# Optimization experiments

Hardware: AMD Instinct MI355X
Metric: run time of the kernel (lower is better)

The kernel has to match this reference:

```python
import jax, jax.numpy as jnp
import numpy as np

E = 1024
H = 16
D = E // H  # head_dim = 64
FF = 4 * E
EPS = 1e-5


def layernorm(x, g, b):
    mu = jnp.mean(x, axis=-1, keepdims=True)
    var = jnp.var(x, axis=-1, keepdims=True)
    return (x - mu) * jax.lax.rsqrt(var + EPS) * g + b


def setup_inputs() -> dict:
    key = jax.random.key(0)
    ks = jax.random.split(key, 12)
    s = 1.0 / np.sqrt(E)
    sf = 1.0 / np.sqrt(FF)
    return {
        "x": jax.random.normal(ks[0], (2, 2048, E), dtype=jnp.float32),
        "wq": jax.random.uniform(ks[1], (E, E), jnp.float32, -s, s),
        "wk": jax.random.uniform(ks[2], (E, E), jnp.float32, -s, s),
        "wv": jax.random.uniform(ks[3], (E, E), jnp.float32, -s, s),
        "wo": jax.random.uniform(ks[4], (E, E), jnp.float32, -s, s),
        "bo": jax.random.uniform(ks[5], (E,), jnp.float32, -s, s),
        "g1": jnp.ones((E,), jnp.float32),
        "b1": jnp.zeros((E,), jnp.float32),
        "w1": jax.random.uniform(ks[6], (FF, E), jnp.float32, -s, s),
        "bf1": jax.random.uniform(ks[7], (FF,), jnp.float32, -s, s),
        "w2": jax.random.uniform(ks[8], (E, FF), jnp.float32, -sf, sf),
        "bf2": jax.random.uniform(ks[9], (E,), jnp.float32, -sf, sf),
        "g2": jnp.ones((E,), jnp.float32),
        "b2": jnp.zeros((E,), jnp.float32),
    }


def reference(x, wq, wk, wv, wo, bo, g1, b1, w1, bf1, w2, bf2, g2, b2):
    B, L, _ = x.shape
    # projections (torch Linear: x @ W.T)
    q = (x @ wq.T).reshape(B, L, H, D).transpose(0, 2, 1, 3)  # (B,H,L,D)
    k = (x @ wk.T).reshape(B, L, H, D).transpose(0, 2, 1, 3)
    v = (x @ wv.T).reshape(B, L, H, D).transpose(0, 2, 1, 3)
    scores = jnp.einsum('bhqd,bhkd->bhqk', q, k) / np.sqrt(D)
    attn = jax.nn.softmax(scores, axis=-1)
    ctx = jnp.einsum('bhqk,bhkd->bhqd', attn, v)
    ctx = ctx.transpose(0, 2, 1, 3).reshape(B, L, E)
    attn_out = ctx @ wo.T + bo
    h = layernorm(x + attn_out, g1, b1)
    ff = jax.nn.gelu(h @ w1.T + bf1, approximate=False) @ w2.T + bf2
    return layernorm(h + ff, g2, b2)
```

## Files before the change

### kernel.cpp

```cpp
#include <hip/hip_runtime.h>
#include <hip/hip_bf16.h>
#include <stdint.h>

typedef __bf16 bf16x8 __attribute__((ext_vector_type(8)));
typedef float  f32x4  __attribute__((ext_vector_type(4)));
typedef unsigned short u16;
typedef u16 u16x8 __attribute__((ext_vector_type(8)));

__device__ __forceinline__ u16 f2b(float f) {
  uint32_t u = __builtin_bit_cast(uint32_t, f);
  u += 0x7fffu + ((u >> 16) & 1u);
  return (u16)(u >> 16);
}

__device__ __forceinline__ float b2f(u16 b) {
  uint32_t u = (uint32_t)b << 16;
  return __builtin_bit_cast(float, u);
}

__device__ __forceinline__ f32x4 mfma16(bf16x8 a, bf16x8 b, f32x4 c) {
  return __builtin_amdgcn_mfma_f32_16x16x32_bf16(a, b, c, 0, 0, 0);
}

__device__ __forceinline__ void gload_lds16(const void* g, void* l) {
  __builtin_amdgcn_global_load_lds(
      (const __attribute__((address_space(1))) void*)g,
      (__attribute__((address_space(3))) void*)l, 16, 0, 0);
}

__global__ void f2b_all(const float* __restrict__ x,  const float* __restrict__ wq,
                        const float* __restrict__ wk, const float* __restrict__ wv,
                        const float* __restrict__ wo, const float* __restrict__ w1,
                        const float* __restrict__ w2,
                        u16* __restrict__ xb, u16* __restrict__ wqkvb,
                        u16* __restrict__ wob, u16* __restrict__ w1b,
                        u16* __restrict__ w2b) {
  const int i = blockIdx.x * blockDim.x + threadIdx.x;
  const float* src; u16* dst; int off;
  if (i < 524288)        { src = x;  dst = xb;              off = i; }
  else if (i < 655360)   { src = wq; dst = wqkvb;           off = i - 524288; }
  else if (i < 786432)   { src = wk; dst = wqkvb + 1048576; off = i - 655360; }
  else if (i < 917504)   { src = wv; dst = wqkvb + 2097152; off = i - 786432; }
  else if (i < 1048576)  { src = wo; dst = wob;             off = i - 917504; }
  else if (i < 1572864)  { src = w1; dst = w1b;             off = i - 1048576; }
  else                   { src = w2; dst = w2b;             off = i - 1572864; }
  const float4* p = (const float4*)src + (size_t)off * 2;
  float4 a = p[0], b = p[1];
  u16x8 r;
  r[0] = f2b(a.x); r[1] = f2b(a.y); r[2] = f2b(a.z); r[3] = f2b(a.w);
  r[4] = f2b(b.x); r[5] = f2b(b.y); r[6] = f2b(b.z); r[7] = f2b(b.w);
  *((u16x8*)dst + off) = r;
}

template<int MODE>
__global__ __launch_bounds__(256, 4) void gemm_bt(
    const u16* __restrict__ A, const u16* __restrict__ W,
    const float* __restrict__ bias,
    void* __restrict__ o0, void* __restrict__ o1,
    void* __restrict__ o2, void* __restrict__ o3,
    int Nsz, int Kstride, int Klen, int ntiles)
{
  __shared__ u16 As[2][128 * 32];
  __shared__ u16 Bs[2][128 * 32];
  const int nbn = Nsz >> 7;
  int bid = blockIdx.x;
  bid = (bid & 7) * ((int)gridDim.x >> 3) + (bid >> 3);
  const int tile = (MODE == 1) ? (bid % ntiles) : bid;
  const int sid  = (MODE == 1) ? (bid / ntiles) : 0;
  const int koff = sid * Klen;
  const int bm = tile / nbn;
  const int bn = tile % nbn;
  const int tid = threadIdx.x;
  const int w = tid >> 6, l = tid & 63;
  const int lh = l >> 4, ll = l & 15;
  const int wr = w >> 1, wc = w & 1;

  f32x4 acc[4][4] = {};

  const u16* Ag = A + (size_t)(bm * 128) * Kstride + koff;
  const u16* Wg = W + (size_t)(bn * 128) * Kstride + koff;

  const int flat0 = (w * 2) * 64 + l;
  const int flat1 = (w * 2 + 1) * 64 + l;

  {
    gload_lds16(Ag + (size_t)(flat0 >> 2) * Kstride + (flat0 & 3) * 8, As[0] + flat0 * 8);
    gload_lds16(Wg + (size_t)(flat0 >> 2) * Kstride + (flat0 & 3) * 8, Bs[0] + flat0 * 8);
    gload_lds16(Ag + (size_t)(flat1 >> 2) * Kstride + (flat1 & 3) * 8, As[0] + flat1 * 8);
    gload_lds16(Wg + (size_t)(flat1 >> 2) * Kstride + (flat1 & 3) * 8, Bs[0] + flat1 * 8);
  }
  __syncthreads();

  const int NS = Klen >> 5;
  int buf = 0;
  for (int s = 0; s < NS; ++s) {
    if (s + 1 < NS) {
      const int k0 = (s + 1) * 32;
      gload_lds16(Ag + (size_t)(flat0 >> 2) * Kstride + k0 + (flat0 & 3) * 8, As[buf ^ 1] + flat0 * 8);
      gload_lds16(Wg + (size_t)(flat0 >> 2) * Kstride + k0 + (flat0 & 3) * 8, Bs[buf ^ 1] + flat0 * 8);
      gload_lds16(Ag + (size_t)(flat1 >> 2) * Kstride + k0 + (flat1 & 3) * 8, As[buf ^ 1] + flat1 * 8);
      gload_lds16(Wg + (size_t)(flat1 >> 2) * Kstride + k0 + (flat1 & 3) * 8, Bs[buf ^ 1] + flat1 * 8);
    }
    bf16x8 af[4], bfr[4];
#pragma unroll
    for (int mi = 0; mi < 4; ++mi)
      af[mi] = *(const bf16x8*)(As[buf] + (wr * 64 + mi * 16 + ll) * 32 + lh * 8);
#pragma unroll
    for (int ni = 0; ni < 4; ++ni)
      bfr[ni] = *(const bf16x8*)(Bs[buf] + (wc * 64 + ni * 16 + ll) * 32 + lh * 8);
    __builtin_amdgcn_s_setprio(1);
#pragma unroll
    for (int mi = 0; mi < 4; ++mi)
#pragma unroll
      for (int ni = 0; ni < 4; ++ni)
        acc[mi][ni] = mfma16(af[mi], bfr[ni], acc[mi][ni]);
    __builtin_amdgcn_s_setprio(0);
    __syncthreads();
    buf ^= 1;
  }

#pragma unroll
  for (int mi = 0; mi < 4; ++mi) {
#pragma unroll
    for (int ni = 0; ni < 4; ++ni) {
      const int col = bn * 128 + wc * 64 + ni * 16 + ll;
#pragma unroll
      for (int i = 0; i < 4; ++i) {
        const int row = bm * 128 + wr * 64 + mi * 16 + lh * 4 + i;
        float v = acc[mi][ni][i];
        if (MODE == 1) {
          u16* dst = (sid == 0) ? (u16*)o0 : (sid == 1) ? (u16*)o1
                   : (sid == 2) ? (u16*)o2 : (u16*)o3;
          dst[(size_t)row * Nsz + col] = f2b(v);
        } else if (MODE == 2) {
          float xx = v + bias[col];
          float u = xx * (0.7978845608f + 0.0356774081f * xx * xx);
          float t = __builtin_amdgcn_exp2f(u * 2.8853900818f);
          float r = __builtin_amdgcn_rcpf(1.0f + t);
          ((u16*)o0)[(size_t)row * Nsz + col] = f2b(xx * t * r);
        } else {
          const int which = col >> 10;
          const int e = col & 1023;
          const int hh = e >> 6, dd = e & 63;
          const int bb = row >> 11, nl = row & 2047;
          if (which == 0) {
            ((u16*)o0)[((size_t)(bb * 16 + hh) * 2048 + nl) * 64 + dd] = f2b(v * 0.18033688f);
          } else if (which == 1) {
            ((u16*)o1)[((size_t)(bb * 16 + hh) * 2048 + nl) * 64 + dd] = f2b(v);
          } else {
            ((u16*)o2)[((size_t)(bb * 16 + hh) * 64 + dd) * 2048 + nl] = f2b(v);
          }
        }
      }
    }
  }
}

__global__ __launch_bounds__(256, 2) void attn_fwd(
    const u16* __restrict__ Q, const u16* __restrict__ K,
    const u16* __restrict__ Vt, u16* __restrict__ ctx)
{
  __shared__ u16 Ks[3][64 * 64];
  __shared__ u16 Vs[3][64 * 64];
  __shared__ u16 Ps[4][32 * 64];

  const int bh = blockIdx.x & 31;
  const int qt = blockIdx.x >> 5;
  const int tid = threadIdx.x;
  const int w = tid >> 6, l = tid & 63;
  const int lh = l >> 4, ll = l & 15;
  const int q0 = qt * 128 + w * 32;

  bf16x8 qf[2][2];
#pragma unroll
  for (int qh = 0; qh < 2; ++qh) {
    const u16* Qg = Q + ((size_t)bh * 2048 + q0 + qh * 16 + ll) * 64;
#pragma unroll
    for (int kk = 0; kk < 2; ++kk)
      qf[qh][kk] = *(const bf16x8*)(Qg + kk * 32 + lh * 8);
  }

  bf16x8 ones;
  {
    const u16 o = 0x3F80;
#pragma unroll
    for (int i = 0; i < 8; ++i) ones[i] = __builtin_bit_cast(__bf16, o);
  }

  f32x4 cacc[2][4] = {};
  f32x4 lacc[2] = {};
  u16* ps = Ps[w];

  const int f0 = tid, f1 = 256 + tid;
  const int r0 = f0 >> 3, s0 = f0 & 7, g0 = (s0 ^ (r0 & 7)) * 8;
  const int r1 = f1 >> 3, s1 = f1 & 7, g1 = (s1 ^ (r1 & 7)) * 8;

  auto stage = [&](int t) {
    const int b = t % 3;
    const int kn = t * 64;
    gload_lds16(K + ((size_t)bh * 2048 + kn + r0) * 64 + g0, Ks[b] + f0 * 8);
    gload_lds16(Vt + ((size_t)bh * 64 + r0) * 2048 + kn + g0, Vs[b] + f0 * 8);
    gload_lds16(K + ((size_t)bh * 2048 + kn + r1) * 64 + g1, Ks[b] + f1 * 8);
    gload_lds16(Vt + ((size_t)bh * 64 + r1) * 2048 + kn + g1, Vs[b] + f1 * 8);
  };

  stage(0); stage(1);
  asm volatile("s_waitcnt vmcnt(4) lgkmcnt(0)" ::: "memory");
  asm volatile("s_barrier" ::: "memory");

  for (int kt = 0; kt < 32; ++kt) {
    const int b = kt % 3;
    if (kt < 30) stage(kt + 2);

    f32x4 st[2][4];
    __builtin_amdgcn_s_setprio(1);
#pragma unroll
    for (int jb = 0; jb < 4; ++jb) {
      f32x4 a0 = {}, a1 = {};
#pragma unroll
      for (int kk = 0; kk < 2; ++kk) {
        const int r = jb * 16 + ll;
        bf16x8 kf = *(const bf16x8*)(Ks[b] + r * 64 + (((kk * 4 + lh) ^ (r & 7)) * 8));
        a0 = mfma16(kf, qf[0][kk], a0);
        a1 = mfma16(kf, qf[1][kk], a1);
      }
      st[0][jb] = a0; st[1][jb] = a1;
    }
    __builtin_amdgcn_s_setprio(0);

#pragma unroll
    for (int qh = 0; qh < 2; ++qh)
#pragma unroll
      for (int jb = 0; jb < 4; ++jb) {
        const float p0 = __builtin_amdgcn_exp2f(st[qh][jb][0]);
        const float p1 = __builtin_amdgcn_exp2f(st[qh][jb][1]);
        const float p2 = __builtin_amdgcn_exp2f(st[qh][jb][2]);
        const float p3 = __builtin_amdgcn_exp2f(st[qh][jb][3]);
        uint2 pk;
        asm("v_cvt_pk_bf16_f32 %0, %1, %2" : "=v"(pk.x) : "v"(p0), "v"(p1));
        asm("v_cvt_pk_bf16_f32 %0, %1, %2" : "=v"(pk.y) : "v"(p2), "v"(p3));
        *(uint2*)(ps + (qh * 16 + ll) * 64 +
                  (((jb * 2 + (lh >> 1)) ^ (ll & 7)) * 8) + (lh & 1) * 4) = pk;
      }

    asm volatile("s_waitcnt lgkmcnt(0)" ::: "memory");
    __builtin_amdgcn_sched_barrier(0);

    __builtin_amdgcn_s_setprio(1);
#pragma unroll
    for (int kk = 0; kk < 2; ++kk) {
      bf16x8 pf0 = *(const bf16x8*)(ps + ll * 64 + (((kk * 4 + lh) ^ (ll & 7)) * 8));
      bf16x8 pf1 = *(const bf16x8*)(ps + (16 + ll) * 64 + (((kk * 4 + lh) ^ (ll & 7)) * 8));
      lacc[0] = mfma16(pf0, ones, lacc[0]);
      lacc[1] = mfma16(pf1, ones, lacc[1]);
#pragma unroll
      for (int db = 0; db < 4; ++db) {
        const int vr = db * 16 + ll;
        bf16x8 vf = *(const bf16x8*)(Vs[b] + vr * 64 + (((kk * 4 + lh) ^ (vr & 7)) * 8));
        cacc[0][db] = mfma16(pf0, vf, cacc[0][db]);
        cacc[1][db] = mfma16(pf1, vf, cacc[1][db]);
      }
    }
    __builtin_amdgcn_s_setprio(0);
    if (kt < 30) asm volatile("s_waitcnt vmcnt(4) lgkmcnt(0)" ::: "memory");
    else         asm volatile("s_waitcnt vmcnt(0) lgkmcnt(0)" ::: "memory");
    asm volatile("s_barrier" ::: "memory");
  }

  const int bb = bh >> 4, hh = bh & 15;
#pragma unroll
  for (int qh = 0; qh < 2; ++qh)
#pragma unroll
    for (int db = 0; db < 4; ++db)
#pragma unroll
      for (int i = 0; i < 4; ++i) {
        const float v = cacc[qh][db][i] / lacc[qh][i];
        const size_t orow = (size_t)bb * 2048 + q0 + qh * 16 + lh * 4 + i;
        const size_t ocol = (size_t)hh * 64 + db * 16 + ll;
        ctx[orow * 1024 + ocol] = f2b(v);
      }
}

__global__ __launch_bounds__(256) void ln_fused(
    const u16* __restrict__ res, const u16* __restrict__ p0,
    const u16* __restrict__ p1,  const u16* __restrict__ p2,
    const u16* __restrict__ p3,  const float* __restrict__ bias,
    const float* __restrict__ g, const float* __restrict__ be,
    float* __restrict__ fo, u16* __restrict__ bo16)
{
  const int row = blockIdx.x;
  const int t = threadIdx.x;
  const size_t base = (size_t)row * 1024 + t * 4;
  float v0, v1, v2, v3;
  {
    ushort4 c = *(const ushort4*)(res + base);
    v0 = b2f(c.x); v1 = b2f(c.y); v2 = b2f(c.z); v3 = b2f(c.w);
  }
  {
    ushort4 c = *(const ushort4*)(p0 + base);
    v0 += b2f(c.x); v1 += b2f(c.y); v2 += b2f(c.z); v3 += b2f(c.w);
  }
  if (p1) {
    ushort4 c = *(const ushort4*)(p1 + base);
    v0 += b2f(c.x); v1 += b2f(c.y); v2 += b2f(c.z); v3 += b2f(c.w);
  }
  if (p2) {
    ushort4 c = *(const ushort4*)(p2 + base);
    v0 += b2f(c.x); v1 += b2f(c.y); v2 += b2f(c.z); v3 += b2f(c.w);
  }
  if (p3) {
    ushort4 c = *(const ushort4*)(p3 + base);
    v0 += b2f(c.x); v1 += b2f(c.y); v2 += b2f(c.z); v3 += b2f(c.w);
  }
  if (bias) {
    float4 xd = *(const float4*)(bias + t * 4);
    v0 += xd.x; v1 += xd.y; v2 += xd.z; v3 += xd.w;
  }
  float s = v0 + v1 + v2 + v3;
  float ss = v0 * v0 + v1 * v1 + v2 * v2 + v3 * v3;
#pragma unroll
  for (int d = 1; d < 64; d <<= 1) {
    s += __shfl_xor(s, d);
    ss += __shfl_xor(ss, d);
  }
  __shared__ float red[8];
  const int w = t >> 6, lid = t & 63;
  if (lid == 0) { red[w] = s; red[4 + w] = ss; }
  __syncthreads();
  s = red[0] + red[1] + red[2] + red[3];
  ss = red[4] + red[5] + red[6] + red[7];
  const float mean = s * (1.0f / 1024.0f);
  const float var = ss * (1.0f / 1024.0f) - mean * mean;
  const float rstd = rsqrtf(var + 1e-5f);
  const float vv[4] = {v0, v1, v2, v3};
#pragma unroll
  for (int i = 0; i < 4; ++i) {
    const int col = t * 4 + i;
    const float hv = (vv[i] - mean) * rstd * g[col] + be[col];
    if (fo) fo[base + i] = hv;
    if (bo16) bo16[base + i] = f2b(hv);
  }
}

extern "C" void kernel_launch(void* const* d_in, const int* in_sizes, int n_in,
                              void* d_out, int out_size, void* d_ws, size_t ws_size,
                              hipStream_t stream) {
  const float* x   = (const float*)d_in[0];
  const float* wq  = (const float*)d_in[1];
  const float* wk  = (const float*)d_in[2];
  const float* wv  = (const float*)d_in[3];
  const float* wo  = (const float*)d_in[4];
  const float* bo  = (const float*)d_in[5];
  const float* g1  = (const float*)d_in[6];
  const float* b1  = (const float*)d_in[7];
  const float* w1  = (const float*)d_in[8];
  const float* bf1 = (const float*)d_in[9];
  const float* w2  = (const float*)d_in[10];
  const float* bf2 = (const float*)d_in[11];
  const float* g2  = (const float*)d_in[12];
  const float* b2  = (const float*)d_in[13];

  char* ws = (char*)d_ws;
  const size_t MB = 1u << 20;
  u16* xb    = (u16*)(ws + 0);
  u16* wqkv  = (u16*)(ws + 8 * MB);
  u16* wob   = (u16*)(ws + 14 * MB);
  u16* w1b   = (u16*)(ws + 16 * MB);
  u16* w2b   = (u16*)(ws + 24 * MB);
  u16* qb    = (u16*)(ws + 32 * MB);
  u16* kb    = (u16*)(ws + 40 * MB);
  u16* vtb   = (u16*)(ws + 48 * MB);
  u16* ctxb  = (u16*)(ws + 56 * MB);
  u16* sp0   = (u16*)(ws + 64 * MB);
  u16* sp1   = (u16*)(ws + 72 * MB);
  u16* sp2   = (u16*)(ws + 80 * MB);
  u16* sp3   = (u16*)(ws + 88 * MB);
  u16* hbb   = (u16*)(ws + 96 * MB);
  u16* ff1   = (u16*)(ws + 32 * MB);

  f2b_all<<<8192, 256, 0, stream>>>(x, wq, wk, wv, wo, w1, w2, xb, wqkv, wob, w1b, w2b);

  gemm_bt<0><<<768, 256, 0, stream>>>(xb, wqkv, nullptr, qb, kb, vtb, nullptr,
                                      3072, 1024, 1024, 768);
  attn_fwd<<<512, 256, 0, stream>>>(qb, kb, vtb, ctxb);
  gemm_bt<1><<<1024, 256, 0, stream>>>(ctxb, wob, nullptr, sp0, sp1, sp2, sp3,
                                       1024, 1024, 256, 256);
  ln_fused<<<4096, 256, 0, stream>>>(xb, sp0, sp1, sp2, sp3, bo, g1, b1,
                                     nullptr, hbb);
  gemm_bt<2><<<1024, 256, 0, stream>>>(hbb, w1b, bf1, ff1, nullptr, nullptr, nullptr,
                                       4096, 1024, 1024, 1024);
  gemm_bt<1><<<1024, 256, 0, stream>>>(ff1, w2b, nullptr, sp0, sp1, sp2, sp3,
                                       1024, 4096, 1024, 256);
  ln_fused<<<4096, 256, 0, stream>>>(hbb, sp0, sp1, sp2, sp3, bf2, g2, b2,
                                     (float*)d_out, nullptr);
}
```

Measured before the change: 242.8 us.

## Software-pipeline QK^T of next tile with softmax and PV of current tile

Restructures the attention inner loop so the QK^T MFMAs for tile t+1 are issued before the exp/pack and PV work of tile t, using two score register sets and a 2x manual unroll. K stays triple-buffered and V drops to double buffering, which cuts LDS use. The aim is to overlap exp/VALU work with matrix ops. In exchange, each step now waits for all outstanding loads (vmcnt(0)) instead of keeping a prefetch in flight, and the extra live score registers may raise register pressure.

```diff
diff --git a/kernel.cpp b/kernel.cpp
--- a/kernel.cpp
+++ b/kernel.cpp
@@ -161,7 +161,7 @@
     const u16* __restrict__ Vt, u16* __restrict__ ctx)
 {
   __shared__ u16 Ks[3][64 * 64];
-  __shared__ u16 Vs[3][64 * 64];
+  __shared__ u16 Vs[2][64 * 64];
   __shared__ u16 Ps[4][32 * 64];
 
   const int bh = blockIdx.x & 31;
@@ -195,24 +195,21 @@
   const int r0 = f0 >> 3, s0 = f0 & 7, g0 = (s0 ^ (r0 & 7)) * 8;
   const int r1 = f1 >> 3, s1 = f1 & 7, g1 = (s1 ^ (r1 & 7)) * 8;
 
-  auto stage = [&](int t) {
+  auto stageK = [&](int t) {
     const int b = t % 3;
     const int kn = t * 64;
     gload_lds16(K + ((size_t)bh * 2048 + kn + r0) * 64 + g0, Ks[b] + f0 * 8);
+    gload_lds16(K + ((size_t)bh * 2048 + kn + r1) * 64 + g1, Ks[b] + f1 * 8);
+  };
+  auto stageV = [&](int t) {
+    const int b = t & 1;
+    const int kn = t * 64;
     gload_lds16(Vt + ((size_t)bh * 64 + r0) * 2048 + kn + g0, Vs[b] + f0 * 8);
-    gload_lds16(K + ((size_t)bh * 2048 + kn + r1) * 64 + g1, Ks[b] + f1 * 8);
     gload_lds16(Vt + ((size_t)bh * 64 + r1) * 2048 + kn + g1, Vs[b] + f1 * 8);
   };
 
-  stage(0); stage(1);
-  asm volatile("s_waitcnt vmcnt(4) lgkmcnt(0)" ::: "memory");
-  asm volatile("s_barrier" ::: "memory");
-
-  for (int kt = 0; kt < 32; ++kt) {
-    const int b = kt % 3;
-    if (kt < 30) stage(kt + 2);
-
-    f32x4 st[2][4];
+  auto qkt = [&](int t, f32x4 (&st)[2][4]) {
+    const u16* Kb = Ks[t % 3];
     __builtin_amdgcn_s_setprio(1);
 #pragma unroll
     for (int jb = 0; jb < 4; ++jb) {
@@ -220,14 +217,16 @@
 #pragma unroll
       for (int kk = 0; kk < 2; ++kk) {
         const int r = jb * 16 + ll;
-        bf16x8 kf = *(const bf16x8*)(Ks[b] + r * 64 + (((kk * 4 + lh) ^ (r & 7)) * 8));
+        bf16x8 kf = *(const bf16x8*)(Kb + r * 64 + (((kk * 4 + lh) ^ (r & 7)) * 8));
         a0 = mfma16(kf, qf[0][kk], a0);
         a1 = mfma16(kf, qf[1][kk], a1);
       }
       st[0][jb] = a0; st[1][jb] = a1;
     }
     __builtin_amdgcn_s_setprio(0);
-
+  };
+
+  auto smax = [&](f32x4 (&st)[2][4]) {
 #pragma unroll
     for (int qh = 0; qh < 2; ++qh)
 #pragma unroll
@@ -242,10 +241,10 @@
         *(uint2*)(ps + (qh * 16 + ll) * 64 +
                   (((jb * 2 + (lh >> 1)) ^ (ll & 7)) * 8) + (lh & 1) * 4) = pk;
       }
-
-    asm volatile("s_waitcnt lgkmcnt(0)" ::: "memory");
-    __builtin_amdgcn_sched_barrier(0);
-
+  };
+
+  auto pv = [&](int t) {
+    const u16* Vb = Vs[t & 1];
     __builtin_amdgcn_s_setprio(1);
 #pragma unroll
     for (int kk = 0; kk < 2; ++kk) {
@@ -256,14 +255,41 @@
 #pragma unroll
       for (int db = 0; db < 4; ++db) {
         const int vr = db * 16 + ll;
-        bf16x8 vf = *(const bf16x8*)(Vs[b] + vr * 64 + (((kk * 4 + lh) ^ (vr & 7)) * 8));
+        bf16x8 vf = *(const bf16x8*)(Vb + vr * 64 + (((kk * 4 + lh) ^ (vr & 7)) * 8));
         cacc[0][db] = mfma16(pf0, vf, cacc[0][db]);
         cacc[1][db] = mfma16(pf1, vf, cacc[1][db]);
       }
     }
     __builtin_amdgcn_s_setprio(0);
-    if (kt < 30) asm volatile("s_waitcnt vmcnt(4) lgkmcnt(0)" ::: "memory");
-    else         asm volatile("s_waitcnt vmcnt(0) lgkmcnt(0)" ::: "memory");
+  };
+
+  stageK(0); stageK(1); stageV(0);
+  asm volatile("s_waitcnt vmcnt(0) lgkmcnt(0)" ::: "memory");
+  asm volatile("s_barrier" ::: "memory");
+
+  f32x4 stA[2][4], stB[2][4];
+  qkt(0, stA);
+
+  for (int kt = 0; kt < 32; kt += 2) {
+    if (kt < 30) stageK(kt + 2);
+    stageV(kt + 1);
+    qkt(kt + 1, stB);
+    smax(stA);
+    asm volatile("s_waitcnt lgkmcnt(0)" ::: "memory");
+    __builtin_amdgcn_sched_barrier(0);
+    pv(kt);
+    asm volatile("s_waitcnt vmcnt(0) lgkmcnt(0)" ::: "memory");
+    asm volatile("s_barrier" ::: "memory");
+
+    const int k2 = kt + 1;
+    if (k2 < 30) stageK(k2 + 2);
+    if (k2 < 31) stageV(k2 + 1);
+    if (k2 < 31) qkt(k2 + 1, stA);
+    smax(stB);
+    asm volatile("s_waitcnt lgkmcnt(0)" ::: "memory");
+    __builtin_amdgcn_sched_barrier(0);
+    pv(k2);
+    asm volatile("s_waitcnt vmcnt(0) lgkmcnt(0)" ::: "memory");
     asm volatile("s_barrier" ::: "memory");
   }
 
```

Measured after the change: 242.1 us. No clear change (-0.3%).
